# Kernel tuning notes

Hardware: AMD Instinct MI355X
Metric: run time of the kernel (lower is better)

The kernel has to match this reference:

```python
import jax, jax.numpy as jnp
import numpy as np

B, T, D, H, NCLS = 256, 512, 75, 512, 11


def setup_inputs() -> dict:
    key = jax.random.key(0)
    ks = jax.random.split(key, 12)
    return {
        "x": jax.random.normal(ks[0], (B, T, D), jnp.float32),
        "w_ih_mu": jax.random.normal(ks[1], (D, 4 * H), jnp.float32) * 0.05,
        "w_ih_rho": jax.random.normal(ks[2], (D, 4 * H), jnp.float32) - 6.0,
        "eps_ih": jax.random.normal(ks[3], (D, 4 * H), jnp.float32),
        "w_hh_mu": jax.random.normal(ks[4], (H, 4 * H), jnp.float32) * 0.05,
        "w_hh_rho": jax.random.normal(ks[5], (H, 4 * H), jnp.float32) - 6.0,
        "eps_hh": jax.random.normal(ks[6], (H, 4 * H), jnp.float32),
        "b_mu": jax.random.normal(ks[7], (4 * H,), jnp.float32) * 0.05,
        "b_rho": jax.random.normal(ks[8], (4 * H,), jnp.float32) - 6.0,
        "eps_b": jax.random.normal(ks[9], (4 * H,), jnp.float32),
        "fc_w": jax.random.normal(ks[10], (NCLS, H), jnp.float32) * 0.05,
        "fc_b": jax.random.normal(ks[11], (NCLS,), jnp.float32) * 0.05,
    }


def reference(x, w_ih_mu, w_ih_rho, eps_ih, w_hh_mu, w_hh_rho, eps_hh,
              b_mu, b_rho, eps_b, fc_w, fc_b):
    # Reparameterized weight sampling (once per forward, as in blitz BayesianLSTM)
    w_ih = w_ih_mu + jax.nn.softplus(w_ih_rho) * eps_ih   # [D, 4H]
    w_hh = w_hh_mu + jax.nn.softplus(w_hh_rho) * eps_hh   # [H, 4H]
    b = b_mu + jax.nn.softplus(b_rho) * eps_b             # [4H]

    batch = x.shape[0]
    h0 = jnp.zeros((batch, H), x.dtype)
    c0 = jnp.zeros((batch, H), x.dtype)

    # Precompute input projection for all timesteps: [T, B, 4H]
    xg = jnp.einsum('btd,dg->tbg', x, w_ih) + b

    def step(carry, xg_t):
        h, c = carry
        gates = xg_t + h @ w_hh                 # [B, 4H]
        i, f, g, o = jnp.split(gates, 4, axis=1)
        c = jax.nn.sigmoid(f) * c + jax.nn.sigmoid(i) * jnp.tanh(g)
        h = jax.nn.sigmoid(o) * jnp.tanh(c)
        return (h, c), None

    (h, c), _ = jax.lax.scan(step, (h0, c0), xg)
    z = h @ fc_w.T + fc_b                       # [B, NCLS]
    return z
```

## Files before the change

kernel.cpp:

```cpp
#include <hip/hip_runtime.h>
#include <hip/hip_bf16.h>

#define T_STEPS 512
#define D_IN 75
#define H_DIM 512
#define G_DIM 2048
#define NCLS_ 11
#define NKK 19
#define NGRP 16
#define NJ 16
#define CH_STRIDE 1536

typedef __attribute__((ext_vector_type(8))) short short8;
typedef __attribute__((ext_vector_type(4))) float f32x4;
typedef __attribute__((ext_vector_type(4))) unsigned int u32x4;

__device__ __forceinline__ unsigned short f2b(float f) {
  unsigned int u = __float_as_uint(f);
  unsigned int r = (u + 0x7fffu + ((u >> 16) & 1u)) >> 16;
  return (unsigned short)r;
}
__device__ __forceinline__ float b2f(unsigned short u) {
  return __uint_as_float(((unsigned int)u) << 16);
}
__device__ __forceinline__ float softplusf(float v) {
  return (v > 20.f) ? v : log1pf(__expf(v));
}
__device__ __forceinline__ float sigmf(float v) {
  return 1.f / (1.f + __expf(-v));
}
__device__ __forceinline__ float tanhf_(float v) {
  float a = fabsf(v);
  float e = __expf(-2.f * a);
  float r = (1.f - e) / (1.f + e);
  return copysignf(r, v);
}
__device__ __forceinline__ unsigned long long pack4(const unsigned short* v) {
  return (unsigned long long)v[0] | ((unsigned long long)v[1] << 16) |
         ((unsigned long long)v[2] << 32) | ((unsigned long long)v[3] << 48);
}

#define ALD(p) __hip_atomic_load((p), __ATOMIC_RELAXED, __HIP_MEMORY_SCOPE_AGENT)
#define AST(p, v) __hip_atomic_store((p), (v), __ATOMIC_RELAXED, __HIP_MEMORY_SCOPE_AGENT)

__global__ __launch_bounds__(64) void pack_w_kernel(
    const float* __restrict__ wih_mu, const float* __restrict__ wih_rho, const float* __restrict__ eps_ih,
    const float* __restrict__ whh_mu, const float* __restrict__ whh_rho, const float* __restrict__ eps_hh,
    unsigned short* __restrict__ wpack)
{
  int c = blockIdx.x;
  int j = c / (8 * NKK);
  int r = c % (8 * NKK);
  int wv = r / NKK;
  int kk = r % NKK;
  int l = threadIdx.x;
  int s = l & 15, grp = l >> 4;
  int q = s >> 2, cc = s & 3;
  int n = q * 512 + j * 32 + wv * 4 + cc;
  unsigned short vs[8];
#pragma unroll
  for (int e = 0; e < 8; ++e) {
    int k = kk * 32 + grp * 8 + e;
    float val = 0.f;
    if (k < 512) {
      int idx = k * G_DIM + n;
      val = whh_mu[idx] + softplusf(whh_rho[idx]) * eps_hh[idx];
    } else if (k < 512 + D_IN) {
      int idx = (k - 512) * G_DIM + n;
      val = wih_mu[idx] + softplusf(wih_rho[idx]) * eps_ih[idx];
    }
    vs[e] = f2b(val);
  }
  unsigned long long u0 = pack4(vs);
  unsigned long long u1 = pack4(vs + 4);
  unsigned long long* dst = (unsigned long long*)wpack + (size_t)c * 128 + l * 2;
  dst[0] = u0;
  dst[1] = u1;
}

__global__ __launch_bounds__(64) void pack_x_kernel(
    const float* __restrict__ x, unsigned short* __restrict__ xpack)
{
  int c = blockIdx.x;
  int t = c >> 3, g = c & 7;
  int lane = threadIdx.x;
  int srow = lane & 15, grp = lane >> 4;
#pragma unroll
  for (int rg = 0; rg < 2; ++rg) {
    const float* xr = x + (size_t)(g * 32 + rg * 16 + srow) * (T_STEPS * D_IN) + (size_t)t * D_IN;
#pragma unroll
    for (int kx = 0; kx < 3; ++kx) {
      unsigned short vs[8];
#pragma unroll
      for (int e = 0; e < 8; ++e) {
        int d = kx * 32 + grp * 8 + e;
        vs[e] = f2b(d < D_IN ? xr[d] : 0.f);
      }
      unsigned long long* dp = (unsigned long long*)xpack +
          ((size_t)(c * 6 + rg * 3 + kx) * 64 + lane) * 2;
      dp[0] = pack4(vs);
      dp[1] = pack4(vs + 4);
    }
  }
}

struct __align__(16) SmemLoop {
  unsigned short hstage[2][16][64][8];
  float gatesT[4][2][16][20];
  unsigned short hq[4][16][8];
};
union Smem {
  SmemLoop s;
  unsigned short zbuf[16][512];
};

template <bool XP>
__global__ __launch_bounds__(256, 1) void lstm_scan_kernel(
    const float* __restrict__ x,
    const unsigned short* __restrict__ wpack,
    const unsigned short* __restrict__ xpack,
    const float* __restrict__ b_mu, const float* __restrict__ b_rho, const float* __restrict__ eps_b,
    const float* __restrict__ fc_w, const float* __restrict__ fc_b,
    char* __restrict__ hbuf, float* __restrict__ out)
{
  __shared__ Smem sm;

  const int bid = blockIdx.x;
  const int g8 = bid & 7;
  const int p = (bid >> 3) & 1;
  const int j = bid >> 4;
  const int gid = g8 * 2 + p;
  const int tid = threadIdx.x;
  const int w = tid >> 6, lane = tid & 63;
  const int srow = lane & 15, grp = lane >> 4;

  short8 Wreg[2][NKK];
  {
    const short8* wp = (const short8*)wpack;
#pragma unroll
    for (int ct = 0; ct < 2; ++ct) {
      const int cj = (j * 8 + w * 2 + ct) * NKK;
#pragma unroll
      for (int kk = 0; kk < NKK; ++kk)
        Wreg[ct][kk] = wp[(size_t)(cj + kk) * 64 + lane];
    }
  }
  float bias_[2][4];
#pragma unroll
  for (int ct = 0; ct < 2; ++ct)
#pragma unroll
    for (int q = 0; q < 4; ++q) {
      int idx = q * 512 + j * 32 + (w * 2 + ct) * 4 + grp;
      bias_[ct][q] = b_mu[idx] + softplusf(b_rho[idx]) * eps_b[idx];
    }

  float cst[2] = {0.f, 0.f};

  float xraw[3][8];
  if constexpr (!XP) {
    const float* xr = x + (size_t)(gid * 16 + srow) * (T_STEPS * D_IN);
#pragma unroll
    for (int kx = 0; kx < 3; ++kx)
#pragma unroll
      for (int e = 0; e < 8; ++e) {
        int d = kx * 32 + grp * 8 + e;
        xraw[kx][e] = (d < D_IN) ? xr[d] : 0.f;
      }
  }

  {
    char* gp0 = hbuf + (size_t)(0 * NGRP + gid) * 16 * CH_STRIDE;
    if (lane < 16) {
      char* cb = gp0 + (size_t)j * CH_STRIDE + (size_t)(w * 16 + lane) * 8;
      AST((unsigned long long*)(cb), 0ull);
      AST((unsigned long long*)(cb + 512), 0ull);
      AST((unsigned long long*)(cb + 1024), 0ull);
    }
  }

  for (int t = 0; t < T_STEPS; ++t) {
    const int par = t & 1;
    short8 xf[3];

    if constexpr (XP) {
      const short8* xp = (const short8*)xpack +
          ((size_t)((t * 8 + g8) * 6 + p * 3)) * 64 + lane;
#pragma unroll
      for (int kx = 0; kx < 3; ++kx)
        xf[kx] = xp[kx * 64];
    }

    const char* gp = hbuf + (size_t)(par * NGRP + gid) * 16 * CH_STRIDE;
    unsigned long long pw[4][3];
    {
      const unsigned long long tgt = (unsigned long long)t;
      while (true) {
#pragma unroll
        for (int c4 = 0; c4 < 4; ++c4) {
          const char* cb = gp + (size_t)(w * 4 + c4) * CH_STRIDE + (size_t)lane * 8;
          pw[c4][0] = ALD((const unsigned long long*)(cb));
          pw[c4][1] = ALD((const unsigned long long*)(cb + 512));
          pw[c4][2] = ALD((const unsigned long long*)(cb + 1024));
        }
        bool ok = true;
#pragma unroll
        for (int c4 = 0; c4 < 4; ++c4)
#pragma unroll
          for (int wd = 0; wd < 3; ++wd)
            ok &= ((pw[c4][wd] >> 48) == tgt);
        if (__all(ok)) break;
        __builtin_amdgcn_s_sleep(1);
      }
    }

    if constexpr (!XP) {
#pragma unroll
      for (int kx = 0; kx < 3; ++kx) {
        unsigned short vs[8];
#pragma unroll
        for (int e = 0; e < 8; ++e) vs[e] = f2b(xraw[kx][e]);
        union { unsigned long long u[2]; short8 v; } q;
        q.u[0] = pack4(vs);
        q.u[1] = pack4(vs + 4);
        xf[kx] = q.v;
      }
    }

#pragma unroll
    for (int c4 = 0; c4 < 4; ++c4) {
      unsigned long long w0 = pw[c4][0], w1 = pw[c4][1], w2 = pw[c4][2];
      unsigned long long lo = (w0 & 0x0000FFFFFFFFFFFFull) | (w1 << 48);
      unsigned long long hi = ((w1 >> 16) & 0xFFFFFFFFull) | ((w2 & 0xFFFFFFFFull) << 32);
      union { unsigned long long u[2]; u32x4 q; } fq;
      fq.u[0] = lo;
      fq.u[1] = hi;
      *(u32x4*)&sm.s.hstage[par][w * 4 + c4][lane][0] = fq.q;
    }

    if constexpr (!XP) {
      if (t + 1 < T_STEPS) {
        const float* xr = x + (size_t)(gid * 16 + srow) * (T_STEPS * D_IN) + (size_t)(t + 1) * D_IN;
#pragma unroll
        for (int kx = 0; kx < 3; ++kx)
#pragma unroll
          for (int e = 0; e < 8; ++e) {
            int d = kx * 32 + grp * 8 + e;
            xraw[kx][e] = (d < D_IN) ? xr[d] : 0.f;
          }
      }
    }

    __syncthreads();

    f32x4 acc[2];
    acc[0] = (f32x4){0.f, 0.f, 0.f, 0.f};
    acc[1] = (f32x4){0.f, 0.f, 0.f, 0.f};
#pragma unroll
    for (int kx = 0; kx < 3; ++kx) {
      acc[0] = __builtin_amdgcn_mfma_f32_16x16x32_bf16(xf[kx], Wreg[0][16 + kx], acc[0], 0, 0, 0);
      acc[1] = __builtin_amdgcn_mfma_f32_16x16x32_bf16(xf[kx], Wreg[1][16 + kx], acc[1], 0, 0, 0);
    }
#pragma unroll
    for (int kk = 0; kk < 16; ++kk) {
      short8 a = *(const short8*)&sm.s.hstage[par][kk][lane][0];
      acc[0] = __builtin_amdgcn_mfma_f32_16x16x32_bf16(a, Wreg[0][kk], acc[0], 0, 0, 0);
      acc[1] = __builtin_amdgcn_mfma_f32_16x16x32_bf16(a, Wreg[1][kk], acc[1], 0, 0, 0);
    }

#pragma unroll
    for (int ct = 0; ct < 2; ++ct)
      *(f32x4*)&sm.s.gatesT[w][ct][srow][grp * 4] = acc[ct];
#pragma unroll
    for (int ct = 0; ct < 2; ++ct) {
      float vi = sm.s.gatesT[w][ct][grp + 0][srow] + bias_[ct][0];
      float vf = sm.s.gatesT[w][ct][grp + 4][srow] + bias_[ct][1];
      float vg = sm.s.gatesT[w][ct][grp + 8][srow] + bias_[ct][2];
      float vo = sm.s.gatesT[w][ct][grp + 12][srow] + bias_[ct][3];
      float ii = sigmf(vi), ff = sigmf(vf);
      float gg = tanhf_(vg), oo = sigmf(vo);
      float cn = ff * cst[ct] + ii * gg;
      cst[ct] = cn;
      float hh = oo * tanhf_(cn);
      sm.s.hq[w][srow][ct * 4 + grp] = f2b(hh);
    }

    {
      char* gpn = hbuf + (size_t)(((t + 1) & 1) * NGRP + gid) * 16 * CH_STRIDE;
      if (lane < 16) {
        const unsigned long long* hp = (const unsigned long long*)&sm.s.hq[w][lane][0];
        unsigned long long a = hp[0], b = hp[1];
        unsigned long long st = ((unsigned long long)(t + 1)) << 48;
        unsigned long long w0 = (a & 0x0000FFFFFFFFFFFFull) | st;
        unsigned long long w1 = ((a >> 48) | ((b & 0xFFFFFFFFull) << 16)) | st;
        unsigned long long w2 = ((b >> 32) & 0xFFFFFFFFull) | st;
        char* cb = gpn + (size_t)j * CH_STRIDE + (size_t)(w * 16 + lane) * 8;
        AST((unsigned long long*)(cb), w0);
        AST((unsigned long long*)(cb + 512), w1);
        AST((unsigned long long*)(cb + 1024), w2);
      }
    }
  }

  if (j == 0) {
    __syncthreads();
    const char* gp0 = hbuf + (size_t)(0 * NGRP + gid) * 16 * CH_STRIDE;
    unsigned long long pw[4][3];
    {
      const unsigned long long tgt = (unsigned long long)T_STEPS;
      while (true) {
#pragma unroll
        for (int c4 = 0; c4 < 4; ++c4) {
          const char* cb = gp0 + (size_t)(w * 4 + c4) * CH_STRIDE + (size_t)lane * 8;
          pw[c4][0] = ALD((const unsigned long long*)(cb));
          pw[c4][1] = ALD((const unsigned long long*)(cb + 512));
          pw[c4][2] = ALD((const unsigned long long*)(cb + 1024));
        }
        bool ok = true;
#pragma unroll
        for (int c4 = 0; c4 < 4; ++c4)
#pragma unroll
          for (int wd = 0; wd < 3; ++wd)
            ok &= ((pw[c4][wd] >> 48) == tgt);
        if (__all(ok)) break;
        __builtin_amdgcn_s_sleep(1);
      }
    }
#pragma unroll
    for (int c4 = 0; c4 < 4; ++c4) {
      unsigned long long w0 = pw[c4][0], w1 = pw[c4][1], w2 = pw[c4][2];
      unsigned long long lo = (w0 & 0x0000FFFFFFFFFFFFull) | (w1 << 48);
      unsigned long long hi = ((w1 >> 16) & 0xFFFFFFFFull) | ((w2 & 0xFFFFFFFFull) << 32);
      int kk = w * 4 + c4;
      int row = lane & 15, k0 = kk * 32 + (lane >> 4) * 8;
      union { unsigned long long u[2]; u32x4 q; } fq;
      fq.u[0] = lo;
      fq.u[1] = hi;
      *(u32x4*)&sm.zbuf[row][k0] = fq.q;
    }
    __syncthreads();
    for (int i = tid; i < 16 * NCLS_; i += 256) {
      int r = i / NCLS_, n = i % NCLS_;
      float s = fc_b[n];
      const float* fw = fc_w + n * H_DIM;
      for (int k = 0; k < H_DIM; ++k)
        s += b2f(sm.zbuf[r][k]) * fw[k];
      out[(gid * 16 + r) * NCLS_ + n] = s;
    }
  }
}

extern "C" void kernel_launch(void* const* d_in, const int* in_sizes, int n_in,
                              void* d_out, int out_size, void* d_ws, size_t ws_size,
                              hipStream_t stream) {
  const float* x       = (const float*)d_in[0];
  const float* wih_mu  = (const float*)d_in[1];
  const float* wih_rho = (const float*)d_in[2];
  const float* eps_ih  = (const float*)d_in[3];
  const float* whh_mu  = (const float*)d_in[4];
  const float* whh_rho = (const float*)d_in[5];
  const float* eps_hh  = (const float*)d_in[6];
  const float* b_mu    = (const float*)d_in[7];
  const float* b_rho   = (const float*)d_in[8];
  const float* eps_b   = (const float*)d_in[9];
  const float* fc_w    = (const float*)d_in[10];
  const float* fc_b    = (const float*)d_in[11];

  unsigned short* wpack = (unsigned short*)d_ws;
  char* hbuf = (char*)d_ws + 2490368;
  unsigned short* xpack = (unsigned short*)((char*)d_ws + 3276800);
  const bool use_xpack = (ws_size >= 3276800ull + 25165824ull);

  hipMemsetAsync(hbuf, 0xFF, 2 * NGRP * 16 * CH_STRIDE, stream);
  pack_w_kernel<<<NJ * 8 * NKK, 64, 0, stream>>>(wih_mu, wih_rho, eps_ih,
                                                 whh_mu, whh_rho, eps_hh, wpack);
  if (use_xpack) {
    pack_x_kernel<<<T_STEPS * 8, 64, 0, stream>>>(x, xpack);
    lstm_scan_kernel<true><<<NGRP * NJ, 256, 0, stream>>>(
        x, wpack, xpack, b_mu, b_rho, eps_b, fc_w, fc_b, hbuf, (float*)d_out);
  } else {
    lstm_scan_kernel<false><<<NGRP * NJ, 256, 0, stream>>>(
        x, wpack, (const unsigned short*)nullptr, b_mu, b_rho, eps_b,
        fc_w, fc_b, hbuf, (float*)d_out);
  }
}
```

Baseline: 1.310 ms.

## Load full hidden state per wave from global, dropping LDS staging and barrier

Each wave now polls and loads all 16 hidden-state chunks directly from the global exchange buffer into registers instead of loading a quarter, staging it through shared memory, and synchronising the block. This removes the LDS round trip and one __syncthreads per timestep. In exchange every wave issues four times as many atomic global loads per step and holds 48 extra 64-bit values in registers, which raises register pressure and L2 traffic in the latency-critical polling loop.

```diff
diff --git a/kernel.cpp b/kernel.cpp
--- a/kernel.cpp
+++ b/kernel.cpp
@@ -105,7 +105,6 @@
 }
 
 struct __align__(16) SmemLoop {
-  unsigned short hstage[2][16][64][8];
   float gatesT[4][2][16][20];
   unsigned short hq[4][16][8];
 };
@@ -191,23 +190,23 @@
     }
 
     const char* gp = hbuf + (size_t)(par * NGRP + gid) * 16 * CH_STRIDE;
-    unsigned long long pw[4][3];
+    unsigned long long pw[16][3];
     {
       const unsigned long long tgt = (unsigned long long)t;
       while (true) {
 #pragma unroll
-        for (int c4 = 0; c4 < 4; ++c4) {
-          const char* cb = gp + (size_t)(w * 4 + c4) * CH_STRIDE + (size_t)lane * 8;
-          pw[c4][0] = ALD((const unsigned long long*)(cb));
-          pw[c4][1] = ALD((const unsigned long long*)(cb + 512));
-          pw[c4][2] = ALD((const unsigned long long*)(cb + 1024));
+        for (int c16 = 0; c16 < 16; ++c16) {
+          const char* cb = gp + (size_t)c16 * CH_STRIDE + (size_t)lane * 8;
+          pw[c16][0] = ALD((const unsigned long long*)(cb));
+          pw[c16][1] = ALD((const unsigned long long*)(cb + 512));
+          pw[c16][2] = ALD((const unsigned long long*)(cb + 1024));
         }
         bool ok = true;
 #pragma unroll
-        for (int c4 = 0; c4 < 4; ++c4)
+        for (int c16 = 0; c16 < 16; ++c16)
 #pragma unroll
           for (int wd = 0; wd < 3; ++wd)
-            ok &= ((pw[c4][wd] >> 48) == tgt);
+            ok &= ((pw[c16][wd] >> 48) == tgt);
         if (__all(ok)) break;
         __builtin_amdgcn_s_sleep(1);
       }
@@ -226,17 +225,6 @@
       }
     }
 
-#pragma unroll
-    for (int c4 = 0; c4 < 4; ++c4) {
-      unsigned long long w0 = pw[c4][0], w1 = pw[c4][1], w2 = pw[c4][2];
-      unsigned long long lo = (w0 & 0x0000FFFFFFFFFFFFull) | (w1 << 48);
-      unsigned long long hi = ((w1 >> 16) & 0xFFFFFFFFull) | ((w2 & 0xFFFFFFFFull) << 32);
-      union { unsigned long long u[2]; u32x4 q; } fq;
-      fq.u[0] = lo;
-      fq.u[1] = hi;
-      *(u32x4*)&sm.s.hstage[par][w * 4 + c4][lane][0] = fq.q;
-    }
-
     if constexpr (!XP) {
       if (t + 1 < T_STEPS) {
         const float* xr = x + (size_t)(gid * 16 + srow) * (T_STEPS * D_IN) + (size_t)(t + 1) * D_IN;
@@ -250,8 +238,6 @@
       }
     }
 
-    __syncthreads();
-
     f32x4 acc[2];
     acc[0] = (f32x4){0.f, 0.f, 0.f, 0.f};
     acc[1] = (f32x4){0.f, 0.f, 0.f, 0.f};
@@ -262,9 +248,14 @@
     }
 #pragma unroll
     for (int kk = 0; kk < 16; ++kk) {
-      short8 a = *(const short8*)&sm.s.hstage[par][kk][lane][0];
-      acc[0] = __builtin_amdgcn_mfma_f32_16x16x32_bf16(a, Wreg[0][kk], acc[0], 0, 0, 0);
-      acc[1] = __builtin_amdgcn_mfma_f32_16x16x32_bf16(a, Wreg[1][kk], acc[1], 0, 0, 0);
+      unsigned long long w0 = pw[kk][0], w1 = pw[kk][1], w2 = pw[kk][2];
+      unsigned long long lo = (w0 & 0x0000FFFFFFFFFFFFull) | (w1 << 48);
+      unsigned long long hi = ((w1 >> 16) & 0xFFFFFFFFull) | ((w2 & 0xFFFFFFFFull) << 32);
+      union { unsigned long long u[2]; short8 v; } q;
+      q.u[0] = lo;
+      q.u[1] = hi;
+      acc[0] = __builtin_amdgcn_mfma_f32_16x16x32_bf16(q.v, Wreg[0][kk], acc[0], 0, 0, 0);
+      acc[1] = __builtin_amdgcn_mfma_f32_16x16x32_bf16(q.v, Wreg[1][kk], acc[1], 0, 0, 0);
     }
 
 #pragma unroll
```

After: 2.504 ms. 1.91x slower.
